# Optimization experiments

Hardware: AMD Instinct MI355X
Metric: run time of the kernel (lower is better)

Reference implementation:

```python
import jax, jax.numpy as jnp
import numpy as np

VOC_QUANT = (100, 100, 50)   # prod = 500_000
EMB_QUANT = (8, 16)          # prod = 128
RANK = 32
TARGET_STD = np.sqrt(2.0 / np.prod(VOC_QUANT))


def setup_inputs() -> dict:
    key = jax.random.key(0)
    ks = jax.random.split(key, 6)
    voc = int(np.prod(VOC_QUANT))
    x = jax.random.randint(ks[0], (1024, 200), 0, voc, dtype=jnp.int64 if jax.config.jax_enable_x64 else jnp.int32).astype(jnp.int32)
    # CP factors, one per tensorized dim; 'nn' init scales so full table std ~ target_stddev
    n_dims = len(VOC_QUANT) + len(EMB_QUANT)
    scale = (TARGET_STD ** (1.0 / n_dims)) / (RANK ** (0.5 / n_dims))
    U0 = jax.random.normal(ks[1], (VOC_QUANT[0], RANK), dtype=jnp.float32) * scale
    U1 = jax.random.normal(ks[2], (VOC_QUANT[1], RANK), dtype=jnp.float32) * scale
    U2 = jax.random.normal(ks[3], (VOC_QUANT[2], RANK), dtype=jnp.float32) * scale
    V0 = jax.random.normal(ks[4], (EMB_QUANT[0], RANK), dtype=jnp.float32) * scale
    V1 = jax.random.normal(ks[5], (EMB_QUANT[1], RANK), dtype=jnp.float32) * scale
    return {"x": x, "U0": U0, "U1": U1, "U2": U2, "V0": V0, "V1": V1}


def reference(x, U0, U1, U2, V0, V1):
    # CP full reconstruction: full[a,b,c,d,e] = sum_r U0[a,r]U1[b,r]U2[c,r]V0[d,r]V1[e,r]
    # reshaped to [voc_size, emb_size], then row gather (matches module's get_full + full[x]).
    voc = U0.shape[0] * U1.shape[0] * U2.shape[0]
    emb = V0.shape[0] * V1.shape[0]
    # Khatri-Rao along rank for vocab factors -> [voc, R]
    A = jnp.einsum('ar,br,cr->abcr', U0, U1, U2).reshape(voc, RANK)
    # Khatri-Rao for embedding factors -> [emb, R]
    B = jnp.einsum('dr,er->der', V0, V1).reshape(emb, RANK)
    full = A @ B.T                    # [voc, emb] dense table (256 MB)
    xshape = x.shape
    rows = full[x.reshape(-1)]        # row gather
    return rows.reshape(*xshape, emb)
```

## Files before the change

### kernel.cpp

```cpp
#include <hip/hip_runtime.h>
#include <hip/hip_bf16.h>


#define RANKK 32
#define EMB 128
#define WAVES_PER_BLOCK 4

typedef __attribute__((ext_vector_type(8))) short short8v;
typedef __attribute__((ext_vector_type(4))) float f32x4;

__device__ __forceinline__ short f2bf(float f) {
    union { __hip_bfloat16 h; short s; } u;
    u.h = __float2bfloat16(f);
    return u.s;
}

__global__ __launch_bounds__(256) void cpemb_mfma(
    const int* __restrict__ x,
    const float* __restrict__ U0, const float* __restrict__ U1,
    const float* __restrict__ U2,
    const float* __restrict__ V0, const float* __restrict__ V1,
    float* __restrict__ out, int ntok)
{
    const int tid  = threadIdx.x;
    const int lane = tid & 63;
    const int gwave  = blockIdx.x * WAVES_PER_BLOCK + (tid >> 6);
    const int nwaves = gridDim.x * WAVES_PER_BLOCK;

    const int t_l = lane & 15;
    const int g   = lane >> 4;
    const int rb  = g * 8;

    float v1r[8];
    {
        const float4* p = (const float4*)(V1 + t_l * RANKK + rb);
        float4 lo = p[0], hi = p[1];
        v1r[0]=lo.x; v1r[1]=lo.y; v1r[2]=lo.z; v1r[3]=lo.w;
        v1r[4]=hi.x; v1r[5]=hi.y; v1r[6]=hi.z; v1r[7]=hi.w;
    }
    short8v bfrag[8];
    #pragma unroll
    for (int eb = 0; eb < 8; ++eb) {
        const float4* p = (const float4*)(V0 + eb * RANKK + rb);
        float4 lo = p[0], hi = p[1];
        float v0r[8] = {lo.x, lo.y, lo.z, lo.w, hi.x, hi.y, hi.z, hi.w};
        #pragma unroll
        for (int i = 0; i < 8; ++i)
            bfrag[eb][i] = f2bf(v0r[i] * v1r[i]);
    }

    const int ngroups = (ntok + 15) >> 4;
    for (int grp = gwave; grp < ngroups; grp += nwaves) {
        const int t0 = grp << 4;

        int tok = t0 + t_l;
        if (tok >= ntok) tok = ntok - 1;
        const unsigned ui  = (unsigned)x[tok];
        const unsigned a   = ui / 5000u;
        const unsigned rem = ui - a * 5000u;
        const unsigned b   = rem / 50u;
        const unsigned c   = rem - b * 50u;

        const float4* p0 = (const float4*)(U0 + a * RANKK + rb);
        const float4* p1 = (const float4*)(U1 + b * RANKK + rb);
        const float4* p2 = (const float4*)(U2 + c * RANKK + rb);
        float4 a0 = p0[0], a1 = p0[1];
        float4 b0 = p1[0], b1 = p1[1];
        float4 c0 = p2[0], c1 = p2[1];
        float wv[8];
        wv[0]=a0.x*b0.x*c0.x; wv[1]=a0.y*b0.y*c0.y;
        wv[2]=a0.z*b0.z*c0.z; wv[3]=a0.w*b0.w*c0.w;
        wv[4]=a1.x*b1.x*c1.x; wv[5]=a1.y*b1.y*c1.y;
        wv[6]=a1.z*b1.z*c1.z; wv[7]=a1.w*b1.w*c1.w;
        short8v afrag;
        #pragma unroll
        for (int i = 0; i < 8; ++i) afrag[i] = f2bf(wv[i]);

        const bool ok = (t0 + t_l) < ntok;
        float* orow = out + (size_t)(t0 + t_l) * EMB + g * 4;
        #pragma unroll
        for (int eb = 0; eb < 8; ++eb) {
            f32x4 acc = {0.f, 0.f, 0.f, 0.f};
            acc = __builtin_amdgcn_mfma_f32_16x16x32_bf16(bfrag[eb], afrag, acc, 0, 0, 0);
            if (ok) {
                float4 v = make_float4(acc[0], acc[1], acc[2], acc[3]);
                *(float4*)(orow + eb * 16) = v;
            }
        }
    }
}

extern "C" void kernel_launch(void* const* d_in, const int* in_sizes, int n_in,
                              void* d_out, int out_size, void* d_ws, size_t ws_size,
                              hipStream_t stream) {
    const int*   x  = (const int*)d_in[0];
    const float* U0 = (const float*)d_in[1];
    const float* U1 = (const float*)d_in[2];
    const float* U2 = (const float*)d_in[3];
    const float* V0 = (const float*)d_in[4];
    const float* V1 = (const float*)d_in[5];
    float* out = (float*)d_out;

    const int ntok = in_sizes[0];
    const int blocks = 1024;

    cpemb_mfma<<<blocks, 256, 0, stream>>>(x, U0, U1, U2, V0, V1, out, ntok);
}
```

Measured before the change: 29.29 us.

## Prefetch next token group's indices and factor rows, transpose MFMA output stores

Turns the grid-stride loop into a software pipeline. Each iteration loads the next group's token index and U0/U1/U2 factor rows while the current group's MFMAs and stores run, so gather latency is hidden. The MFMA operand order is swapped, so each lane now writes scalar floats with lanes contiguous along the embedding dimension, instead of one float4 per lane. It also adds an occupancy hint of 6 blocks in launch_bounds and raises the grid from 1024 to 1536 blocks. Costs are more store instructions and extra registers held for the prefetch.

```diff
diff --git a/kernel.cpp b/kernel.cpp
--- a/kernel.cpp
+++ b/kernel.cpp
@@ -4,7 +4,6 @@
 
 #define RANKK 32
 #define EMB 128
-#define WAVES_PER_BLOCK 4
 
 typedef __attribute__((ext_vector_type(8))) short short8v;
 typedef __attribute__((ext_vector_type(4))) float f32x4;
@@ -15,7 +14,7 @@
     return u.s;
 }
 
-__global__ __launch_bounds__(256) void cpemb_mfma(
+__global__ __launch_bounds__(256, 6) void cpemb_mfma(
     const int* __restrict__ x,
     const float* __restrict__ U0, const float* __restrict__ U1,
     const float* __restrict__ U2,
@@ -24,8 +23,9 @@
 {
     const int tid  = threadIdx.x;
     const int lane = tid & 63;
-    const int gwave  = blockIdx.x * WAVES_PER_BLOCK + (tid >> 6);
-    const int nwaves = gridDim.x * WAVES_PER_BLOCK;
+    const int gw   = blockIdx.x * 4 + (tid >> 6);
+    const int nw   = gridDim.x * 4;
+    const int ngroups = (ntok + 15) >> 4;
 
     const int t_l = lane & 15;
     const int g   = lane >> 4;
@@ -49,43 +49,78 @@
             bfrag[eb][i] = f2bf(v0r[i] * v1r[i]);
     }
 
-    const int ngroups = (ntok + 15) >> 4;
-    for (int grp = gwave; grp < ngroups; grp += nwaves) {
-        const int t0 = grp << 4;
+    int grp = gw;
+    if (grp >= ngroups) return;
 
-        int tok = t0 + t_l;
+    float4 ua0, ua1, ub0, ub1, uc0, uc1;
+    {
+        int tok = (grp << 4) + t_l;
         if (tok >= ntok) tok = ntok - 1;
         const unsigned ui  = (unsigned)x[tok];
         const unsigned a   = ui / 5000u;
         const unsigned rem = ui - a * 5000u;
         const unsigned b   = rem / 50u;
         const unsigned c   = rem - b * 50u;
-
         const float4* p0 = (const float4*)(U0 + a * RANKK + rb);
         const float4* p1 = (const float4*)(U1 + b * RANKK + rb);
         const float4* p2 = (const float4*)(U2 + c * RANKK + rb);
-        float4 a0 = p0[0], a1 = p0[1];
-        float4 b0 = p1[0], b1 = p1[1];
-        float4 c0 = p2[0], c1 = p2[1];
+        ua0 = p0[0]; ua1 = p0[1];
+        ub0 = p1[0]; ub1 = p1[1];
+        uc0 = p2[0]; uc1 = p2[1];
+    }
+    int nxt = grp + nw;
+    unsigned ui_n = 0u;
+    if (nxt < ngroups) {
+        int tn = (nxt << 4) + t_l;
+        if (tn >= ntok) tn = ntok - 1;
+        ui_n = (unsigned)x[tn];
+    }
+
+    while (true) {
         float wv[8];
-        wv[0]=a0.x*b0.x*c0.x; wv[1]=a0.y*b0.y*c0.y;
-        wv[2]=a0.z*b0.z*c0.z; wv[3]=a0.w*b0.w*c0.w;
-        wv[4]=a1.x*b1.x*c1.x; wv[5]=a1.y*b1.y*c1.y;
-        wv[6]=a1.z*b1.z*c1.z; wv[7]=a1.w*b1.w*c1.w;
+        wv[0]=ua0.x*ub0.x*uc0.x; wv[1]=ua0.y*ub0.y*uc0.y;
+        wv[2]=ua0.z*ub0.z*uc0.z; wv[3]=ua0.w*ub0.w*uc0.w;
+        wv[4]=ua1.x*ub1.x*uc1.x; wv[5]=ua1.y*ub1.y*uc1.y;
+        wv[6]=ua1.z*ub1.z*uc1.z; wv[7]=ua1.w*ub1.w*uc1.w;
         short8v afrag;
         #pragma unroll
         for (int i = 0; i < 8; ++i) afrag[i] = f2bf(wv[i]);
 
+        const bool have_nxt = nxt < ngroups;
+        if (have_nxt) {
+            const unsigned a   = ui_n / 5000u;
+            const unsigned rem = ui_n - a * 5000u;
+            const unsigned b   = rem / 50u;
+            const unsigned c   = rem - b * 50u;
+            const float4* p0 = (const float4*)(U0 + a * RANKK + rb);
+            const float4* p1 = (const float4*)(U1 + b * RANKK + rb);
+            const float4* p2 = (const float4*)(U2 + c * RANKK + rb);
+            ua0 = p0[0]; ua1 = p0[1];
+            ub0 = p1[0]; ub1 = p1[1];
+            uc0 = p2[0]; uc1 = p2[1];
+        }
+
+        const int t0 = grp << 4;
         const bool ok = (t0 + t_l) < ntok;
-        float* orow = out + (size_t)(t0 + t_l) * EMB + g * 4;
+        float* ob = out + (size_t)(t0 + g * 4) * EMB + t_l;
         #pragma unroll
         for (int eb = 0; eb < 8; ++eb) {
-            f32x4 acc = {0.f, 0.f, 0.f, 0.f};
-            acc = __builtin_amdgcn_mfma_f32_16x16x32_bf16(bfrag[eb], afrag, acc, 0, 0, 0);
+            f32x4 z = {0.f, 0.f, 0.f, 0.f};
+            f32x4 acc = __builtin_amdgcn_mfma_f32_16x16x32_bf16(afrag, bfrag[eb], z, 0, 0, 0);
             if (ok) {
-                float4 v = make_float4(acc[0], acc[1], acc[2], acc[3]);
-                *(float4*)(orow + eb * 16) = v;
+                #pragma unroll
+                for (int j = 0; j < 4; ++j)
+                    ob[(size_t)j * EMB + eb * 16] = acc[j];
             }
+        }
+
+        if (!have_nxt) break;
+        grp = nxt;
+        nxt = grp + nw;
+        if (nxt < ngroups) {
+            int tn = (nxt << 4) + t_l;
+            if (tn >= ntok) tn = ntok - 1;
+            ui_n = (unsigned)x[tn];
         }
     }
 }
@@ -102,7 +137,7 @@
     float* out = (float*)d_out;
 
     const int ntok = in_sizes[0];
-    const int blocks = 1024;
+    const int blocks = 1536;
 
     cpemb_mfma<<<blocks, 256, 0, stream>>>(x, U0, U1, U2, V0, V1, out, ntok);
 }
```

Measured after the change: 55.70 us. 1.9x slower.

## Stage MFMA outputs through LDS for coalesced stores and prefetch token indices

Applied to the files above, without the earlier changes.

Each wave now writes its 16x128 MFMA output tile into a padded LDS buffer and then reads it back so that consecutive lanes store consecutive 16-byte chunks of the output, giving fully contiguous global writes. The grid-stride loop is replaced by a fixed unrolled loop of four groups per wave, and all four token indices are loaded up front to hide index-load latency. The LDS round trip adds shared-memory traffic and requires a wave-local ordering between the write and the read. The fixed four-iteration bound assumes the grid times four covers all groups, which holds for the current sizes but silently drops tokens otherwise.

```diff
diff --git a/kernel.cpp b/kernel.cpp
--- a/kernel.cpp
+++ b/kernel.cpp
@@ -4,7 +4,7 @@
 
 #define RANKK 32
 #define EMB 128
-#define WAVES_PER_BLOCK 4
+#define LDSW 132
 
 typedef __attribute__((ext_vector_type(8))) short short8v;
 typedef __attribute__((ext_vector_type(4))) float f32x4;
@@ -22,14 +22,31 @@
     const float* __restrict__ V0, const float* __restrict__ V1,
     float* __restrict__ out, int ntok)
 {
+    __shared__ float stile[4][16 * LDSW];
+
     const int tid  = threadIdx.x;
     const int lane = tid & 63;
-    const int gwave  = blockIdx.x * WAVES_PER_BLOCK + (tid >> 6);
-    const int nwaves = gridDim.x * WAVES_PER_BLOCK;
+    const int wv_i = tid >> 6;
+    const int gw   = blockIdx.x * 4 + wv_i;
+    const int nw   = gridDim.x * 4;
+    const int ngroups = (ntok + 15) >> 4;
 
     const int t_l = lane & 15;
     const int g   = lane >> 4;
     const int rb  = g * 8;
+
+    float* my = &stile[wv_i][0];
+
+    unsigned ui[4];
+    bool has[4];
+    #pragma unroll
+    for (int k = 0; k < 4; ++k) {
+        const int grp = gw + k * nw;
+        has[k] = grp < ngroups;
+        int tok = (grp << 4) + t_l;
+        if (tok >= ntok) tok = ntok - 1;
+        ui[k] = (unsigned)x[tok];
+    }
 
     float v1r[8];
     {
@@ -49,42 +66,56 @@
             bfrag[eb][i] = f2bf(v0r[i] * v1r[i]);
     }
 
-    const int ngroups = (ntok + 15) >> 4;
-    for (int grp = gwave; grp < ngroups; grp += nwaves) {
-        const int t0 = grp << 4;
+    #pragma unroll
+    for (int k = 0; k < 4; ++k) {
+        if (!has[k]) break;
+        const int grp = gw + k * nw;
+        const int t0  = grp << 4;
 
-        int tok = t0 + t_l;
-        if (tok >= ntok) tok = ntok - 1;
-        const unsigned ui  = (unsigned)x[tok];
-        const unsigned a   = ui / 5000u;
-        const unsigned rem = ui - a * 5000u;
+        const unsigned u   = ui[k];
+        const unsigned a   = u / 5000u;
+        const unsigned rem = u - a * 5000u;
         const unsigned b   = rem / 50u;
         const unsigned c   = rem - b * 50u;
-
         const float4* p0 = (const float4*)(U0 + a * RANKK + rb);
         const float4* p1 = (const float4*)(U1 + b * RANKK + rb);
         const float4* p2 = (const float4*)(U2 + c * RANKK + rb);
         float4 a0 = p0[0], a1 = p0[1];
         float4 b0 = p1[0], b1 = p1[1];
         float4 c0 = p2[0], c1 = p2[1];
-        float wv[8];
-        wv[0]=a0.x*b0.x*c0.x; wv[1]=a0.y*b0.y*c0.y;
-        wv[2]=a0.z*b0.z*c0.z; wv[3]=a0.w*b0.w*c0.w;
-        wv[4]=a1.x*b1.x*c1.x; wv[5]=a1.y*b1.y*c1.y;
-        wv[6]=a1.z*b1.z*c1.z; wv[7]=a1.w*b1.w*c1.w;
+        float wvv[8];
+        wvv[0]=a0.x*b0.x*c0.x; wvv[1]=a0.y*b0.y*c0.y;
+        wvv[2]=a0.z*b0.z*c0.z; wvv[3]=a0.w*b0.w*c0.w;
+        wvv[4]=a1.x*b1.x*c1.x; wvv[5]=a1.y*b1.y*c1.y;
+        wvv[6]=a1.z*b1.z*c1.z; wvv[7]=a1.w*b1.w*c1.w;
         short8v afrag;
         #pragma unroll
-        for (int i = 0; i < 8; ++i) afrag[i] = f2bf(wv[i]);
+        for (int i = 0; i < 8; ++i) afrag[i] = f2bf(wvv[i]);
 
-        const bool ok = (t0 + t_l) < ntok;
-        float* orow = out + (size_t)(t0 + t_l) * EMB + g * 4;
         #pragma unroll
         for (int eb = 0; eb < 8; ++eb) {
-            f32x4 acc = {0.f, 0.f, 0.f, 0.f};
-            acc = __builtin_amdgcn_mfma_f32_16x16x32_bf16(bfrag[eb], afrag, acc, 0, 0, 0);
-            if (ok) {
-                float4 v = make_float4(acc[0], acc[1], acc[2], acc[3]);
-                *(float4*)(orow + eb * 16) = v;
+            f32x4 z = {0.f, 0.f, 0.f, 0.f};
+            f32x4 acc = __builtin_amdgcn_mfma_f32_16x16x32_bf16(bfrag[eb], afrag, z, 0, 0, 0);
+            float4 v = make_float4(acc[0], acc[1], acc[2], acc[3]);
+            *(float4*)&my[t_l * LDSW + eb * 16 + g * 4] = v;
+        }
+
+        if (t0 + 16 <= ntok) {
+            #pragma unroll
+            for (int s = 0; s < 8; ++s) {
+                const int fo = s * 256 + lane * 4;
+                float4 v = *(const float4*)&my[(fo >> 7) * LDSW + (fo & 127)];
+                *(float4*)&out[(size_t)t0 * EMB + fo] = v;
+            }
+        } else {
+            #pragma unroll
+            for (int s = 0; s < 8; ++s) {
+                const int fo = s * 256 + lane * 4;
+                const int t  = fo >> 7;
+                if (t0 + t < ntok) {
+                    float4 v = *(const float4*)&my[t * LDSW + (fo & 127)];
+                    *(float4*)&out[(size_t)t0 * EMB + fo] = v;
+                }
             }
         }
     }
```

New measurement: 27.58 us. -5.8%, faster.

## Split CP embedding into weight-gather kernel and MFMA expand kernel

Applied to the files above, without the earlier changes.

Splits the fused kernel in two. The first kernel gathers the three vocab factor rows per token and writes their bf16 Khatri-Rao product to workspace. The second kernel loads these bf16 vectors up front, TPW groups per wave, and expands them with MFMA against the V0⊙V1 fragments. The aim is to take the dependent gather latency out of the store-bound expand loop and batch loads. The cost is a second launch and an extra round trip of the intermediate through global memory.

```diff
diff --git a/kernel.cpp b/kernel.cpp
--- a/kernel.cpp
+++ b/kernel.cpp
@@ -4,7 +4,7 @@
 
 #define RANKK 32
 #define EMB 128
-#define WAVES_PER_BLOCK 4
+#define TPW 4
 
 typedef __attribute__((ext_vector_type(8))) short short8v;
 typedef __attribute__((ext_vector_type(4))) float f32x4;
@@ -15,21 +15,73 @@
     return u.s;
 }
 
-__global__ __launch_bounds__(256) void cpemb_mfma(
+__global__ __launch_bounds__(256) void cpemb_w(
     const int* __restrict__ x,
     const float* __restrict__ U0, const float* __restrict__ U1,
     const float* __restrict__ U2,
+    short* __restrict__ w, int ntok)
+{
+    const int tid  = threadIdx.x;
+    const int lane = tid & 63;
+    const int base = blockIdx.x * 64 + (tid >> 6) * 16;
+    const int t_l  = lane & 15;
+    const int g    = lane >> 4;
+    const int rb   = g * 8;
+
+    int tok = base + t_l;
+    const bool ok = tok < ntok;
+    if (!ok) tok = ntok - 1;
+
+    const unsigned ui  = (unsigned)x[tok];
+    const unsigned a   = ui / 5000u;
+    const unsigned rem = ui - a * 5000u;
+    const unsigned b   = rem / 50u;
+    const unsigned c   = rem - b * 50u;
+
+    const float4* p0 = (const float4*)(U0 + a * RANKK + rb);
+    const float4* p1 = (const float4*)(U1 + b * RANKK + rb);
+    const float4* p2 = (const float4*)(U2 + c * RANKK + rb);
+    float4 a0 = p0[0], a1 = p0[1];
+    float4 b0 = p1[0], b1 = p1[1];
+    float4 c0 = p2[0], c1 = p2[1];
+
+    float wv[8];
+    wv[0]=a0.x*b0.x*c0.x; wv[1]=a0.y*b0.y*c0.y;
+    wv[2]=a0.z*b0.z*c0.z; wv[3]=a0.w*b0.w*c0.w;
+    wv[4]=a1.x*b1.x*c1.x; wv[5]=a1.y*b1.y*c1.y;
+    wv[6]=a1.z*b1.z*c1.z; wv[7]=a1.w*b1.w*c1.w;
+
+    short8v sv;
+    #pragma unroll
+    for (int i = 0; i < 8; ++i) sv[i] = f2bf(wv[i]);
+
+    if (ok)
+        *(short8v*)(w + (size_t)tok * RANKK + rb) = sv;
+}
+
+__global__ __launch_bounds__(256) void cpemb_expand(
+    const short* __restrict__ w,
     const float* __restrict__ V0, const float* __restrict__ V1,
     float* __restrict__ out, int ntok)
 {
     const int tid  = threadIdx.x;
     const int lane = tid & 63;
-    const int gwave  = blockIdx.x * WAVES_PER_BLOCK + (tid >> 6);
-    const int nwaves = gridDim.x * WAVES_PER_BLOCK;
+    const int gw   = blockIdx.x * 4 + (tid >> 6);
+    const int t_l  = lane & 15;
+    const int g    = lane >> 4;
+    const int rb   = g * 8;
 
-    const int t_l = lane & 15;
-    const int g   = lane >> 4;
-    const int rb  = g * 8;
+    const int grp0    = gw * TPW;
+    const int ngroups = (ntok + 15) >> 4;
+    if (grp0 >= ngroups) return;
+
+    short8v af[TPW];
+    #pragma unroll
+    for (int k = 0; k < TPW; ++k) {
+        int grp = grp0 + k;
+        if (grp >= ngroups) grp = ngroups - 1;
+        af[k] = *(const short8v*)(w + ((size_t)(grp * 16 + t_l)) * RANKK + rb);
+    }
 
     float v1r[8];
     {
@@ -49,39 +101,17 @@
             bfrag[eb][i] = f2bf(v0r[i] * v1r[i]);
     }
 
-    const int ngroups = (ntok + 15) >> 4;
-    for (int grp = gwave; grp < ngroups; grp += nwaves) {
+    #pragma unroll
+    for (int k = 0; k < TPW; ++k) {
+        const int grp = grp0 + k;
+        if (grp >= ngroups) break;
         const int t0 = grp << 4;
-
-        int tok = t0 + t_l;
-        if (tok >= ntok) tok = ntok - 1;
-        const unsigned ui  = (unsigned)x[tok];
-        const unsigned a   = ui / 5000u;
-        const unsigned rem = ui - a * 5000u;
-        const unsigned b   = rem / 50u;
-        const unsigned c   = rem - b * 50u;
-
-        const float4* p0 = (const float4*)(U0 + a * RANKK + rb);
-        const float4* p1 = (const float4*)(U1 + b * RANKK + rb);
-        const float4* p2 = (const float4*)(U2 + c * RANKK + rb);
-        float4 a0 = p0[0], a1 = p0[1];
-        float4 b0 = p1[0], b1 = p1[1];
-        float4 c0 = p2[0], c1 = p2[1];
-        float wv[8];
-        wv[0]=a0.x*b0.x*c0.x; wv[1]=a0.y*b0.y*c0.y;
-        wv[2]=a0.z*b0.z*c0.z; wv[3]=a0.w*b0.w*c0.w;
-        wv[4]=a1.x*b1.x*c1.x; wv[5]=a1.y*b1.y*c1.y;
-        wv[6]=a1.z*b1.z*c1.z; wv[7]=a1.w*b1.w*c1.w;
-        short8v afrag;
-        #pragma unroll
-        for (int i = 0; i < 8; ++i) afrag[i] = f2bf(wv[i]);
-
         const bool ok = (t0 + t_l) < ntok;
         float* orow = out + (size_t)(t0 + t_l) * EMB + g * 4;
         #pragma unroll
         for (int eb = 0; eb < 8; ++eb) {
-            f32x4 acc = {0.f, 0.f, 0.f, 0.f};
-            acc = __builtin_amdgcn_mfma_f32_16x16x32_bf16(bfrag[eb], afrag, acc, 0, 0, 0);
+            f32x4 z = {0.f, 0.f, 0.f, 0.f};
+            f32x4 acc = __builtin_amdgcn_mfma_f32_16x16x32_bf16(bfrag[eb], af[k], z, 0, 0, 0);
             if (ok) {
                 float4 v = make_float4(acc[0], acc[1], acc[2], acc[3]);
                 *(float4*)(orow + eb * 16) = v;
@@ -100,9 +130,15 @@
     const float* V0 = (const float*)d_in[4];
     const float* V1 = (const float*)d_in[5];
     float* out = (float*)d_out;
+    short* w   = (short*)d_ws;
 
     const int ntok = in_sizes[0];
-    const int blocks = 1024;
+    const int ngroups = (ntok + 15) >> 4;
 
-    cpemb_mfma<<<blocks, 256, 0, stream>>>(x, U0, U1, U2, V0, V1, out, ntok);
+    const int blocksA = (ntok + 63) >> 6;
+    cpemb_w<<<blocksA, 256, 0, stream>>>(x, U0, U1, U2, w, ntok);
+
+    const int nwaves  = (ngroups + TPW - 1) / TPW;
+    const int blocksB = (nwaves + 3) >> 2;
+    cpemb_expand<<<blocksB, 256, 0, stream>>>(w, V0, V1, out, ntok);
 }
```

Result: slower. 42.85 us (+46.3%).
